# Kernel tuning notes

Hardware: AMD Instinct MI355X
Metric: run time of the kernel (lower is better)

The kernel has to match this reference:

```python
import jax, jax.numpy as jnp
import numpy as np

N_NODES = 50000
NEG_SLOPE = 0.2


def gat_conv(x, src, dst, W, att_src, att_dst, bias, concat):
    # x: [N, F_in], W: [H*D, F_in], att_*: [H, D], bias: [H*D] or [D]
    N = x.shape[0]
    H, D = att_src.shape
    h = (x @ W.T).reshape(N, H, D)                      # [N, H, D]
    a_src = jnp.einsum('nhd,hd->nh', h, att_src)        # [N, H]
    a_dst = jnp.einsum('nhd,hd->nh', h, att_dst)        # [N, H]
    e = jax.nn.leaky_relu(a_src[src] + a_dst[dst], NEG_SLOPE)  # [E, H]
    # softmax over incoming edges of each destination node
    m = jax.ops.segment_max(e, dst, num_segments=N)     # [N, H]
    ex = jnp.exp(e - m[dst])
    denom = jax.ops.segment_sum(ex, dst, num_segments=N)
    alpha = ex / denom[dst]                             # [E, H]
    msg = alpha[:, :, None] * h[src]                    # [E, H, D]
    out = jax.ops.segment_sum(msg, dst, num_segments=N) # [N, H, D]
    out = out.reshape(N, H * D) if concat else out.mean(axis=1)
    return out + bias


def setup_inputs() -> dict:
    key = jax.random.key(0)
    ks = jax.random.split(key, 10)
    nfeat, nhid, nclass, heads = 256, 128, 40, 4
    d1 = nhid // heads  # 32
    E = 800000
    x = jax.random.normal(ks[0], (N_NODES, nfeat), dtype=jnp.float32)
    edge_index = jax.random.randint(ks[1], (2, E), 0, N_NODES, dtype=jnp.int64)
    s = 0.1
    W1 = jax.random.normal(ks[2], (heads * d1, nfeat), dtype=jnp.float32) * s
    att_src1 = jax.random.normal(ks[3], (heads, d1), dtype=jnp.float32) * s
    att_dst1 = jax.random.normal(ks[4], (heads, d1), dtype=jnp.float32) * s
    b1 = jnp.zeros((heads * d1,), dtype=jnp.float32)
    W2 = jax.random.normal(ks[5], (nclass, nhid), dtype=jnp.float32) * s
    att_src2 = jax.random.normal(ks[6], (1, nclass), dtype=jnp.float32) * s
    att_dst2 = jax.random.normal(ks[7], (1, nclass), dtype=jnp.float32) * s
    b2 = jnp.zeros((nclass,), dtype=jnp.float32)
    return {"x": x, "edge_index": edge_index, "W1": W1, "att_src1": att_src1,
            "att_dst1": att_dst1, "b1": b1, "W2": W2, "att_src2": att_src2,
            "att_dst2": att_dst2, "b2": b2}


def reference(x, edge_index, W1, att_src1, att_dst1, b1, W2, att_src2, att_dst2, b2):
    # PyG GATConv adds self-loops by default
    loops = jnp.arange(N_NODES, dtype=edge_index.dtype)
    src = jnp.concatenate([edge_index[0], loops])
    dst = jnp.concatenate([edge_index[1], loops])
    h = gat_conv(x, src, dst, W1, att_src1, att_dst1, b1, concat=True)
    h = jax.nn.relu(h)
    # dropout is identity in eval mode
    out = gat_conv(h, src, dst, W2, att_src2, att_dst2, b2, concat=True)
    return out
```

## Files before the change

kernel.cpp:

```cpp
#include <hip/hip_runtime.h>
#include <hip/hip_bf16.h>
#include <cstdint>
#include <cstddef>

#define N_NODES 50000
#define NEG_SLOPE 0.2f
#define NB 196
#define BIN_CHUNK 8192
#define SLICE_MAX 14336

typedef float floatx4 __attribute__((ext_vector_type(4)));
typedef short shortx8 __attribute__((ext_vector_type(8)));

__device__ __forceinline__ unsigned short f2b(float f) {
    union { float f; unsigned u; } v; v.f = f;
    unsigned u = v.u;
    return (unsigned short)((u + 0x7FFFu + ((u >> 16) & 1u)) >> 16);
}
__device__ __forceinline__ float b2f(unsigned short b) {
    union { unsigned u; float f; } v; v.u = ((unsigned)b) << 16;
    return v.f;
}

__global__ __launch_bounds__(256) void bucket_hist_kernel(
    const int* __restrict__ ei, int E0, int E, int* __restrict__ bhist,
    int* __restrict__ bhist_blk) {
    __shared__ int h[NB];
    int t = threadIdx.x;
    for (int i = t; i < NB; i += 256) h[i] = 0;
    __syncthreads();
    int base = blockIdx.x * BIN_CHUNK;
    int end = min(base + BIN_CHUNK, E);
    for (int e = base + t; e < end; e += 256) {
        int d = (e < E0) ? ei[E0 + e] : (e - E0);
        atomicAdd(&h[d >> 8], 1);
    }
    __syncthreads();
    for (int i = t; i < NB; i += 256) {
        int c = h[i];
        bhist_blk[blockIdx.x * NB + i] = c;
        if (c) atomicAdd(&bhist[i], c);
    }
}

__global__ __launch_bounds__(256) void bucket_scan_kernel(
    const int* __restrict__ bhist, int* __restrict__ bbase,
    int* __restrict__ bcursor, int* __restrict__ rowptr, int E) {
    __shared__ int buf[256];
    int t = threadIdx.x;
    int v = (t < NB) ? bhist[t] : 0;
    int x = v;
    for (int off = 1; off < 256; off <<= 1) {
        buf[t] = x; __syncthreads();
        int y = (t >= off) ? buf[t - off] : 0;
        __syncthreads();
        x += y;
    }
    if (t < NB) {
        bbase[t] = x - v;
        bcursor[t] = x - v;
    }
    if (t == NB - 1) bbase[NB] = x;
    if (t == 0) rowptr[N_NODES] = E;
}

__global__ __launch_bounds__(256) void bin_kernel(
    const int* __restrict__ ei, int E0, int E,
    int* __restrict__ bcursor, unsigned int* __restrict__ ebuf,
    const int* __restrict__ bhist_blk) {
    __shared__ int h[NB];
    __shared__ int gbase[NB];
    int t = threadIdx.x;
    for (int i = t; i < NB; i += 256) {
        int c = bhist_blk[blockIdx.x * NB + i];
        gbase[i] = c ? atomicAdd(&bcursor[i], c) : 0;
        h[i] = 0;
    }
    __syncthreads();
    int base = blockIdx.x * BIN_CHUNK;
    int end = min(base + BIN_CHUNK, E);
    for (int e = base + t; e < end; e += 256) {
        int s, d;
        if (e < E0) { s = ei[e]; d = ei[E0 + e]; }
        else        { s = e - E0; d = e - E0; }
        int b = d >> 8;
        int off = atomicAdd(&h[b], 1);
        ebuf[gbase[b] + off] = (unsigned)s | ((unsigned)(d & 255) << 16);
    }
}

__global__ __launch_bounds__(256) void build_kernel(
    const unsigned int* __restrict__ ebuf, const int* __restrict__ bbase,
    int* __restrict__ rowptr, int* __restrict__ csr_src) {
    __shared__ int h[256];
    __shared__ int lrp[257];
    __shared__ int stag[SLICE_MAX];
    int b = blockIdx.x, t = threadIdx.x;
    int e0 = bbase[b], e1 = bbase[b + 1];
    int cnt = e1 - e0;
    int n0 = b << 8;
    h[t] = 0;
    __syncthreads();
    for (int i = t; i < cnt; i += 256)
        atomicAdd(&h[ebuf[e0 + i] >> 16], 1);
    __syncthreads();
    int v = h[t], x = v;
    __shared__ int buf[256];
    for (int off = 1; off < 256; off <<= 1) {
        buf[t] = x; __syncthreads();
        int y = (t >= off) ? buf[t - off] : 0;
        __syncthreads();
        x += y;
    }
    lrp[t] = x - v;
    if (t == 255) lrp[256] = x;
    h[t] = 0;
    __syncthreads();
    int n = n0 + t;
    if (n < N_NODES) rowptr[n] = e0 + lrp[t];
    for (int i = t; i < cnt; i += 256) {
        unsigned int v2 = ebuf[e0 + i];
        int dloc = v2 >> 16;
        int off = atomicAdd(&h[dloc], 1);
        stag[lrp[dloc] + off] = (int)(v2 & 0xFFFFu);
    }
    __syncthreads();
    for (int i = t; i < cnt; i += 256) csr_src[e0 + i] = stag[i];
}

template <int BM, int BN, int NREAL, int KK, int HEADS, typename InT>
__global__ __launch_bounds__(256) void gemm_att_kernel(
    const InT* __restrict__ A, const float* __restrict__ B,
    const float* __restrict__ att_src, const float* __restrict__ att_dst,
    unsigned short* __restrict__ Cb, float* __restrict__ a_src,
    float* __restrict__ a_dst, int M) {
    const int BK = 64, LDK = 72;
    const int NT = BN / 16;
    const int MT = BM / 64;
    const int NKI = KK / BK;
    const int LDC = NREAL + 8;
    const int NAf = BM * 16 / 256;
    const int NAs = BM * 8 / 256;
    const int NBv = BN * 16 / 256;
    constexpr int SMEM = ((BM + BN) * LDK > BM * LDC) ? (BM + BN) * LDK : BM * LDC;
    __shared__ unsigned short smem[SMEM];
    unsigned short* As = smem;
    unsigned short* Bs = smem + BM * LDK;
    const int t = threadIdx.x;
    const int wave = t >> 6, lane = t & 63;
    const int lrow = lane & 15, lkg = lane >> 4;
    const int bm = blockIdx.x * BM;

    floatx4 acc[MT][NT] = {};

    float4 avf[(sizeof(InT) == 4) ? NAf : 1];
    shortx8 avs[(sizeof(InT) == 2) ? NAs : 1];
    float4 bv[NBv];

    {
        const int k0 = 0;
        if constexpr (sizeof(InT) == 4) {
#pragma unroll
            for (int q = 0; q < NAf; q++) {
                int i = t + q * 256;
                int r = i >> 4, c4 = (i & 15) << 2;
                int gr = bm + r;
                avf[q] = (gr < M) ? *(const float4*)&A[(size_t)gr * KK + k0 + c4]
                                  : make_float4(0.f, 0.f, 0.f, 0.f);
            }
        } else {
#pragma unroll
            for (int q = 0; q < NAs; q++) {
                int i = t + q * 256;
                int r = i >> 3, c8 = (i & 7) << 3;
                int gr = bm + r;
                shortx8 z = {};
                avs[q] = (gr < M) ? *(const shortx8*)&A[(size_t)gr * KK + k0 + c8] : z;
            }
        }
#pragma unroll
        for (int q = 0; q < NBv; q++) {
            int i = t + q * 256;
            int r = i >> 4, c4 = (i & 15) << 2;
            bv[q] = (r < NREAL) ? *(const float4*)&B[(size_t)r * KK + k0 + c4]
                                : make_float4(0.f, 0.f, 0.f, 0.f);
        }
    }

    for (int ki = 0; ki < NKI; ki++) {
        __syncthreads();
        if constexpr (sizeof(InT) == 4) {
#pragma unroll
            for (int q = 0; q < NAf; q++) {
                int i = t + q * 256;
                int r = i >> 4, c4 = (i & 15) << 2;
                int o = r * LDK + c4;
                float4 v = avf[q];
                As[o] = f2b(v.x); As[o + 1] = f2b(v.y);
                As[o + 2] = f2b(v.z); As[o + 3] = f2b(v.w);
            }
        } else {
#pragma unroll
            for (int q = 0; q < NAs; q++) {
                int i = t + q * 256;
                int r = i >> 3, c8 = (i & 7) << 3;
                *(shortx8*)&As[r * LDK + c8] = avs[q];
            }
        }
#pragma unroll
        for (int q = 0; q < NBv; q++) {
            int i = t + q * 256;
            int r = i >> 4, c4 = (i & 15) << 2;
            int o = r * LDK + c4;
            float4 v = bv[q];
            Bs[o] = f2b(v.x); Bs[o + 1] = f2b(v.y);
            Bs[o + 2] = f2b(v.z); Bs[o + 3] = f2b(v.w);
        }
        if (ki + 1 < NKI) {
            const int k0 = (ki + 1) * BK;
            if constexpr (sizeof(InT) == 4) {
#pragma unroll
                for (int q = 0; q < NAf; q++) {
                    int i = t + q * 256;
                    int r = i >> 4, c4 = (i & 15) << 2;
                    int gr = bm + r;
                    avf[q] = (gr < M) ? *(const float4*)&A[(size_t)gr * KK + k0 + c4]
                                      : make_float4(0.f, 0.f, 0.f, 0.f);
                }
            } else {
#pragma unroll
                for (int q = 0; q < NAs; q++) {
                    int i = t + q * 256;
                    int r = i >> 3, c8 = (i & 7) << 3;
                    int gr = bm + r;
                    shortx8 z = {};
                    avs[q] = (gr < M) ? *(const shortx8*)&A[(size_t)gr * KK + k0 + c8] : z;
                }
            }
#pragma unroll
            for (int q = 0; q < NBv; q++) {
                int i = t + q * 256;
                int r = i >> 4, c4 = (i & 15) << 2;
                bv[q] = (r < NREAL) ? *(const float4*)&B[(size_t)r * KK + k0 + c4]
                                    : make_float4(0.f, 0.f, 0.f, 0.f);
            }
        }
        __syncthreads();
        for (int ks = 0; ks < BK; ks += 32) {
            int kc = ks + lkg * 8;
#pragma unroll
            for (int mt = 0; mt < MT; mt++) {
                int row = wave * (MT * 16) + mt * 16 + lrow;
                shortx8 a = *(const shortx8*)&As[row * LDK + kc];
#pragma unroll
                for (int nt = 0; nt < NT; nt++) {
                    shortx8 b = *(const shortx8*)&Bs[(nt * 16 + lrow) * LDK + kc];
                    acc[mt][nt] = __builtin_amdgcn_mfma_f32_16x16x32_bf16(a, b, acc[mt][nt], 0, 0, 0);
                }
            }
        }
    }

    __syncthreads();
    unsigned short* Cs = smem;
#pragma unroll
    for (int mt = 0; mt < MT; mt++)
#pragma unroll
        for (int nt = 0; nt < NT; nt++)
#pragma unroll
            for (int r = 0; r < 4; r++) {
                int row = wave * (MT * 16) + mt * 16 + lkg * 4 + r;
                int col = nt * 16 + lrow;
                if (col < NREAL) Cs[row * LDC + col] = f2b(acc[mt][nt][r]);
            }
    __syncthreads();

    const int NCH = NREAL / 8;
    for (int i = t; i < BM * NCH; i += 256) {
        int row = i / NCH, ch = i - row * NCH;
        if (bm + row < M)
            *(shortx8*)&Cb[(size_t)(bm + row) * NREAL + ch * 8] =
                *(const shortx8*)&Cs[row * LDC + ch * 8];
    }

    const int D = NREAL / HEADS;
    if (t < 2 * BM) {
        int row = t >> 1, which = t & 1;
        if (bm + row < M) {
            const float* av = which ? att_dst : att_src;
            float hs[HEADS];
#pragma unroll
            for (int h = 0; h < HEADS; h++) hs[h] = 0.f;
#pragma unroll
            for (int c = 0; c < NCH; c++) {
                float4 p = *(const float4*)&av[c * 8];
                float4 q = *(const float4*)&av[c * 8 + 4];
                shortx8 cv = *(const shortx8*)&Cs[row * LDC + c * 8];
                float s = b2f((unsigned short)cv[0]) * p.x
                        + b2f((unsigned short)cv[1]) * p.y
                        + b2f((unsigned short)cv[2]) * p.z
                        + b2f((unsigned short)cv[3]) * p.w
                        + b2f((unsigned short)cv[4]) * q.x
                        + b2f((unsigned short)cv[5]) * q.y
                        + b2f((unsigned short)cv[6]) * q.z
                        + b2f((unsigned short)cv[7]) * q.w;
                hs[(c * 8) / D] += s;
            }
            float* outp = which ? a_dst : a_src;
#pragma unroll
            for (int h = 0; h < HEADS; h++)
                outp[(size_t)(bm + row) * HEADS + h] = hs[h];
        }
    }
}

__global__ __launch_bounds__(256) void agg1_kernel(
    const unsigned short* __restrict__ h1b, const float* __restrict__ a_src,
    const float* __restrict__ a_dst, const int* __restrict__ rowptr,
    const int* __restrict__ csr_src, const float* __restrict__ b1,
    unsigned short* __restrict__ zb, int N) {
    int wave = threadIdx.x >> 6, lane = threadIdx.x & 63;
    int n = blockIdx.x * 4 + wave;
    if (n >= N) return;
    int eg = lane >> 4;
    int fpos = lane & 15;
    int hd = fpos >> 2;
    int lidx = lane >> 2;
    int lh = lane & 3;
    float adn = a_dst[n * 4 + lh];
    int beg = rowptr[n], deg = rowptr[n + 1] - beg;

    float acc[8] = {0.f, 0.f, 0.f, 0.f, 0.f, 0.f, 0.f, 0.f};
    float den = 0.f;

    int s_e = (lidx < deg) ? csr_src[beg + lidx] : 0;
    float asv = a_src[(s_e << 2) + lh];

    for (int c0 = 0; c0 < deg; c0 += 16) {
        float l = asv + adn;
        l = l > 0.f ? l : NEG_SLOPE * l;
        float w_e = (c0 + lidx < deg) ? __expf(l) : 0.f;
        int cnt = min(16, deg - c0);
        int s4[4]; float w4[4]; shortx8 v4[4];
#pragma unroll
        for (int q = 0; q < 4; q++) {
            int el = (q << 2) + eg;
            s4[q] = __shfl(s_e, el << 2);
            w4[q] = __shfl(w_e, (el << 2) + hd);
        }
#pragma unroll
        for (int q = 0; q < 4; q++) {
            if (q * 4 < cnt)
                v4[q] = *(const shortx8*)&h1b[(size_t)s4[q] * 128 + fpos * 8];
        }
        int nidx = c0 + 16 + lidx;
        int s_n = (nidx < deg) ? csr_src[beg + nidx] : 0;
        float asn = a_src[(s_n << 2) + lh];
#pragma unroll
        for (int q = 0; q < 4; q++) {
            if (q * 4 < cnt) {
                float w = w4[q];
                den += w;
#pragma unroll
                for (int j = 0; j < 8; j++)
                    acc[j] += w * b2f((unsigned short)v4[q][j]);
            }
        }
        s_e = s_n; asv = asn;
    }
#pragma unroll
    for (int j = 0; j < 8; j++) {
        acc[j] += __shfl_xor(acc[j], 16);
        acc[j] += __shfl_xor(acc[j], 32);
    }
    den += __shfl_xor(den, 16);
    den += __shfl_xor(den, 32);
    if (lane < 16) {
        float inv = 1.f / den;
        float4 bb0 = *(const float4*)&b1[fpos * 8];
        float4 bb1 = *(const float4*)&b1[fpos * 8 + 4];
        shortx8 r;
        r[0] = (short)f2b(fmaxf(acc[0] * inv + bb0.x, 0.f));
        r[1] = (short)f2b(fmaxf(acc[1] * inv + bb0.y, 0.f));
        r[2] = (short)f2b(fmaxf(acc[2] * inv + bb0.z, 0.f));
        r[3] = (short)f2b(fmaxf(acc[3] * inv + bb0.w, 0.f));
        r[4] = (short)f2b(fmaxf(acc[4] * inv + bb1.x, 0.f));
        r[5] = (short)f2b(fmaxf(acc[5] * inv + bb1.y, 0.f));
        r[6] = (short)f2b(fmaxf(acc[6] * inv + bb1.z, 0.f));
        r[7] = (short)f2b(fmaxf(acc[7] * inv + bb1.w, 0.f));
        *(shortx8*)&zb[(size_t)n * 128 + fpos * 8] = r;
    }
}

__global__ __launch_bounds__(256) void agg2_kernel(
    const unsigned short* __restrict__ h2b, const float* __restrict__ a_src,
    const float* __restrict__ a_dst, const int* __restrict__ rowptr,
    const int* __restrict__ csr_src, const float* __restrict__ b2,
    float* __restrict__ out, int N) {
    int wave = threadIdx.x >> 6, lane = threadIdx.x & 63;
    int n = blockIdx.x * 4 + wave;
    if (n >= N) return;
    int eg = (lane >= 40) ? 2 : (lane >= 20 ? 1 : 0);
    int fp = lane - eg * 20;
    bool act = fp < 20;
    float adn = a_dst[n];
    int beg = rowptr[n], deg = rowptr[n + 1] - beg;

    float2 acc = {0.f, 0.f};
    float den = 0.f;
    for (int c0 = 0; c0 < deg; c0 += 48) {
        int idx = c0 + lane;
        bool cv = (lane < 48) && (idx < deg);
        int s_e = cv ? csr_src[beg + idx] : 0;
        float l = a_src[s_e] + adn;
        l = l > 0.f ? l : NEG_SLOPE * l;
        float w_e = cv ? __expf(l) : 0.f;
        int cnt = min(48, deg - c0);
#pragma unroll
        for (int qq = 0; qq < 4; qq++) {
            if (qq * 12 < cnt) {
                int s4[4]; float w4[4]; ushort2 v4[4];
#pragma unroll
                for (int q = 0; q < 4; q++) {
                    int el = qq * 12 + q * 3 + eg;
                    s4[q] = __shfl(s_e, el);
                    w4[q] = __shfl(w_e, el);
                }
#pragma unroll
                for (int q = 0; q < 4; q++) {
                    if (act)
                        v4[q] = *(const ushort2*)&h2b[(size_t)s4[q] * 40 + fp * 2];
                }
#pragma unroll
                for (int q = 0; q < 4; q++) {
                    float w = w4[q];
                    den += w;
                    if (act) {
                        acc.x += w * b2f(v4[q].x);
                        acc.y += w * b2f(v4[q].y);
                    }
                }
            }
        }
    }
    float a1x = __shfl(acc.x, fp + 20), a2x = __shfl(acc.x, fp + 40);
    float a1y = __shfl(acc.y, fp + 20), a2y = __shfl(acc.y, fp + 40);
    float d1  = __shfl(den,  fp + 20), d2  = __shfl(den,  fp + 40);
    if (lane < 20) {
        float sx = acc.x + a1x + a2x;
        float sy = acc.y + a1y + a2y;
        float dtot = den + d1 + d2;
        float inv = 1.f / dtot;
        float2 bb = *(const float2*)&b2[fp * 2];
        float2 o;
        o.x = sx * inv + bb.x;
        o.y = sy * inv + bb.y;
        *(float2*)&out[(size_t)n * 40 + fp * 2] = o;
    }
}

extern "C" void kernel_launch(void* const* d_in, const int* in_sizes, int n_in,
                              void* d_out, int out_size, void* d_ws, size_t ws_size,
                              hipStream_t stream) {
    const float* x        = (const float*)d_in[0];
    const int*   ei       = (const int*)d_in[1];
    const float* W1       = (const float*)d_in[2];
    const float* att_src1 = (const float*)d_in[3];
    const float* att_dst1 = (const float*)d_in[4];
    const float* b1       = (const float*)d_in[5];
    const float* W2       = (const float*)d_in[6];
    const float* att_src2 = (const float*)d_in[7];
    const float* att_dst2 = (const float*)d_in[8];
    const float* b2       = (const float*)d_in[9];
    float* out = (float*)d_out;

    const int N  = N_NODES;
    const int E0 = in_sizes[1] / 2;
    const int E  = E0 + N;
    const int NBLK = (E + BIN_CHUNK - 1) / BIN_CHUNK;

    char* ws = (char*)d_ws;
    unsigned short* h1b = (unsigned short*)(ws + 0);
    unsigned short* zb  = (unsigned short*)(ws + 12800000);
    unsigned short* h2b = (unsigned short*)(ws + 25600000);
    float* a_src1 = (float*)(ws + 29600000);
    float* a_dst1 = (float*)(ws + 30400000);
    float* a_src2 = (float*)(ws + 31200000);
    float* a_dst2 = (float*)(ws + 31400000);
    int*   rowptr = (int*)(ws + 31600000);
    int*   bhist  = (int*)(ws + 31800192);
    int*   bbase  = (int*)(ws + 31801088);
    int*   bcursor= (int*)(ws + 31801984);
    unsigned int* ebuf = (unsigned int*)(ws + 31802880);
    int*   csr_src= (int*)(ws + 35202880);
    int*   bhist_blk = (int*)(ws + 38602880);

    hipMemsetAsync(bhist, 0, NB * sizeof(int), stream);

    bucket_hist_kernel<<<NBLK, 256, 0, stream>>>(ei, E0, E, bhist, bhist_blk);
    bucket_scan_kernel<<<1, 256, 0, stream>>>(bhist, bbase, bcursor, rowptr, E);
    bin_kernel<<<NBLK, 256, 0, stream>>>(ei, E0, E, bcursor, ebuf, bhist_blk);
    build_kernel<<<NB, 256, 0, stream>>>(ebuf, bbase, rowptr, csr_src);

    gemm_att_kernel<128, 128, 128, 256, 4, float>
        <<<(N + 127) / 128, 256, 0, stream>>>(x, W1, att_src1, att_dst1,
                                              h1b, a_src1, a_dst1, N);
    agg1_kernel<<<(N + 3) / 4, 256, 0, stream>>>(h1b, a_src1, a_dst1, rowptr, csr_src, b1, zb, N);

    gemm_att_kernel<64, 48, 40, 128, 1, unsigned short>
        <<<(N + 63) / 64, 256, 0, stream>>>(zb, W2, att_src2, att_dst2,
                                            h2b, a_src2, a_dst2, N);
    agg2_kernel<<<(N + 3) / 4, 256, 0, stream>>>(h2b, a_src2, a_dst2, rowptr, csr_src, b2, out, N);
}
```

Before: 221.4 us.

## Fuse bucket histogram and scan, simplify bf16 unpack, shrink GEMM1 tile

Merges the bucket histogram and scan kernels into one launch, with the last block to finish (tracked by an atomic counter) doing the column sums and prefix scan. This removes a kernel launch and the global atomics. The bf16-to-float conversion in both aggregation kernels now unpacks 32-bit words with a shift and a mask. The first GEMM uses 64-row tiles, which doubles the number of blocks for better occupancy but reduces reuse within each block.

```diff
diff --git a/kernel.cpp b/kernel.cpp
--- a/kernel.cpp
+++ b/kernel.cpp
@@ -22,9 +22,11 @@
     return v.f;
 }
 
-__global__ __launch_bounds__(256) void bucket_hist_kernel(
-    const int* __restrict__ ei, int E0, int E, int* __restrict__ bhist,
-    int* __restrict__ bhist_blk) {
+__global__ __launch_bounds__(256) void bucket_hist_scan_kernel(
+    const int* __restrict__ ei, int E0, int E,
+    int* __restrict__ bhist_blk, int* __restrict__ done,
+    int* __restrict__ bbase, int* __restrict__ bcursor,
+    int* __restrict__ rowptr) {
     __shared__ int h[NB];
     int t = threadIdx.x;
     for (int i = t; i < NB; i += 256) h[i] = 0;
@@ -36,19 +38,19 @@
         atomicAdd(&h[d >> 8], 1);
     }
     __syncthreads();
-    for (int i = t; i < NB; i += 256) {
-        int c = h[i];
-        bhist_blk[blockIdx.x * NB + i] = c;
-        if (c) atomicAdd(&bhist[i], c);
-    }
-}
-
-__global__ __launch_bounds__(256) void bucket_scan_kernel(
-    const int* __restrict__ bhist, int* __restrict__ bbase,
-    int* __restrict__ bcursor, int* __restrict__ rowptr, int E) {
+    for (int i = t; i < NB; i += 256)
+        bhist_blk[blockIdx.x * NB + i] = h[i];
+    __threadfence();
+    __shared__ int lastFlag;
+    if (t == 0) lastFlag = (atomicAdd(done, 1) == (int)gridDim.x - 1) ? 1 : 0;
+    __syncthreads();
+    if (!lastFlag) return;
+    __threadfence();
+    int v = 0;
+    if (t < NB)
+        for (int blk = 0; blk < (int)gridDim.x; blk++)
+            v += bhist_blk[blk * NB + t];
     __shared__ int buf[256];
-    int t = threadIdx.x;
-    int v = (t < NB) ? bhist[t] : 0;
     int x = v;
     for (int off = 1; off < 256; off <<= 1) {
         buf[t] = x; __syncthreads();
@@ -330,7 +332,7 @@
     float adn = a_dst[n * 4 + lh];
     int beg = rowptr[n], deg = rowptr[n + 1] - beg;
 
-    float acc[8] = {0.f, 0.f, 0.f, 0.f, 0.f, 0.f, 0.f, 0.f};
+    float2 acc2[4] = {{0.f, 0.f}, {0.f, 0.f}, {0.f, 0.f}, {0.f, 0.f}};
     float den = 0.f;
 
     int s_e = (lidx < deg) ? csr_src[beg + lidx] : 0;
@@ -361,17 +363,25 @@
             if (q * 4 < cnt) {
                 float w = w4[q];
                 den += w;
-#pragma unroll
-                for (int j = 0; j < 8; j++)
-                    acc[j] += w * b2f((unsigned short)v4[q][j]);
+                const unsigned* up = (const unsigned*)&v4[q];
+#pragma unroll
+                for (int p = 0; p < 4; p++) {
+                    unsigned u = up[p];
+                    float lo = __uint_as_float(u << 16);
+                    float hi = __uint_as_float(u & 0xffff0000u);
+                    acc2[p].x += w * lo;
+                    acc2[p].y += w * hi;
+                }
             }
         }
         s_e = s_n; asv = asn;
     }
 #pragma unroll
-    for (int j = 0; j < 8; j++) {
-        acc[j] += __shfl_xor(acc[j], 16);
-        acc[j] += __shfl_xor(acc[j], 32);
+    for (int p = 0; p < 4; p++) {
+        acc2[p].x += __shfl_xor(acc2[p].x, 16);
+        acc2[p].x += __shfl_xor(acc2[p].x, 32);
+        acc2[p].y += __shfl_xor(acc2[p].y, 16);
+        acc2[p].y += __shfl_xor(acc2[p].y, 32);
     }
     den += __shfl_xor(den, 16);
     den += __shfl_xor(den, 32);
@@ -380,14 +390,14 @@
         float4 bb0 = *(const float4*)&b1[fpos * 8];
         float4 bb1 = *(const float4*)&b1[fpos * 8 + 4];
         shortx8 r;
-        r[0] = (short)f2b(fmaxf(acc[0] * inv + bb0.x, 0.f));
-        r[1] = (short)f2b(fmaxf(acc[1] * inv + bb0.y, 0.f));
-        r[2] = (short)f2b(fmaxf(acc[2] * inv + bb0.z, 0.f));
-        r[3] = (short)f2b(fmaxf(acc[3] * inv + bb0.w, 0.f));
-        r[4] = (short)f2b(fmaxf(acc[4] * inv + bb1.x, 0.f));
-        r[5] = (short)f2b(fmaxf(acc[5] * inv + bb1.y, 0.f));
-        r[6] = (short)f2b(fmaxf(acc[6] * inv + bb1.z, 0.f));
-        r[7] = (short)f2b(fmaxf(acc[7] * inv + bb1.w, 0.f));
+        r[0] = (short)f2b(fmaxf(acc2[0].x * inv + bb0.x, 0.f));
+        r[1] = (short)f2b(fmaxf(acc2[0].y * inv + bb0.y, 0.f));
+        r[2] = (short)f2b(fmaxf(acc2[1].x * inv + bb0.z, 0.f));
+        r[3] = (short)f2b(fmaxf(acc2[1].y * inv + bb0.w, 0.f));
+        r[4] = (short)f2b(fmaxf(acc2[2].x * inv + bb1.x, 0.f));
+        r[5] = (short)f2b(fmaxf(acc2[2].y * inv + bb1.y, 0.f));
+        r[6] = (short)f2b(fmaxf(acc2[3].x * inv + bb1.z, 0.f));
+        r[7] = (short)f2b(fmaxf(acc2[3].y * inv + bb1.w, 0.f));
         *(shortx8*)&zb[(size_t)n * 128 + fpos * 8] = r;
     }
 }
@@ -419,7 +429,7 @@
 #pragma unroll
         for (int qq = 0; qq < 4; qq++) {
             if (qq * 12 < cnt) {
-                int s4[4]; float w4[4]; ushort2 v4[4];
+                int s4[4]; float w4[4]; unsigned u4[4];
 #pragma unroll
                 for (int q = 0; q < 4; q++) {
                     int el = qq * 12 + q * 3 + eg;
@@ -429,15 +439,17 @@
 #pragma unroll
                 for (int q = 0; q < 4; q++) {
                     if (act)
-                        v4[q] = *(const ushort2*)&h2b[(size_t)s4[q] * 40 + fp * 2];
+                        u4[q] = *(const unsigned*)&h2b[(size_t)s4[q] * 40 + fp * 2];
                 }
 #pragma unroll
                 for (int q = 0; q < 4; q++) {
                     float w = w4[q];
                     den += w;
                     if (act) {
-                        acc.x += w * b2f(v4[q].x);
-                        acc.y += w * b2f(v4[q].y);
+                        float lo = __uint_as_float(u4[q] << 16);
+                        float hi = __uint_as_float(u4[q] & 0xffff0000u);
+                        acc.x += w * lo;
+                        acc.y += w * hi;
                     }
                 }
             }
@@ -488,23 +500,23 @@
     float* a_src2 = (float*)(ws + 31200000);
     float* a_dst2 = (float*)(ws + 31400000);
     int*   rowptr = (int*)(ws + 31600000);
-    int*   bhist  = (int*)(ws + 31800192);
+    int*   done   = (int*)(ws + 31800192);
     int*   bbase  = (int*)(ws + 31801088);
     int*   bcursor= (int*)(ws + 31801984);
     unsigned int* ebuf = (unsigned int*)(ws + 31802880);
     int*   csr_src= (int*)(ws + 35202880);
     int*   bhist_blk = (int*)(ws + 38602880);
 
-    hipMemsetAsync(bhist, 0, NB * sizeof(int), stream);
-
-    bucket_hist_kernel<<<NBLK, 256, 0, stream>>>(ei, E0, E, bhist, bhist_blk);
-    bucket_scan_kernel<<<1, 256, 0, stream>>>(bhist, bbase, bcursor, rowptr, E);
+    hipMemsetAsync(done, 0, sizeof(int), stream);
+
+    bucket_hist_scan_kernel<<<NBLK, 256, 0, stream>>>(ei, E0, E, bhist_blk,
+                                                      done, bbase, bcursor, rowptr);
     bin_kernel<<<NBLK, 256, 0, stream>>>(ei, E0, E, bcursor, ebuf, bhist_blk);
     build_kernel<<<NB, 256, 0, stream>>>(ebuf, bbase, rowptr, csr_src);
 
-    gemm_att_kernel<128, 128, 128, 256, 4, float>
-        <<<(N + 127) / 128, 256, 0, stream>>>(x, W1, att_src1, att_dst1,
-                                              h1b, a_src1, a_dst1, N);
+    gemm_att_kernel<64, 128, 128, 256, 4, float>
+        <<<(N + 63) / 64, 256, 0, stream>>>(x, W1, att_src1, att_dst1,
+                                            h1b, a_src1, a_dst1, N);
     agg1_kernel<<<(N + 3) / 4, 256, 0, stream>>>(h1b, a_src1, a_dst1, rowptr, csr_src, b1, zb, N);
 
     gemm_att_kernel<64, 48, 40, 128, 1, unsigned short>
```

After: 238.9 us. 1.08x slower.
